# Optimization experiments

Measured on AMD Instinct MI355X. Metric: run time of the kernel, lower is better.

The kernel has to match this reference:

```python
import jax, jax.numpy as jnp
import numpy as np

D = 128          # embedding_dim
H = 8            # attention heads
DH = D // H      # per-head dim
SPLIT = 50000    # hyper-edge zero rows prepended
NX = 150000      # input node feature rows
N0 = SPLIT + NX  # layer-0 source nodes
N1 = 50000       # layer-0 targets
N2 = 30000       # layer-1 targets
N3 = 10000       # layer-2 targets
E0, E1, E2 = 500000, 300000, 100000
NTYPE = 65       # e_num + 1 edge types
NEG_SLOPE = 0.2
BETA = 0.5       # residual_beta (learn_beta=False)
BN_EPS = 1e-5

WEIGHT_NAMES = ['Wq0','Wk0','Wv0','Ws0','Wq1','Wk1','Wv1','Ws1','Wek1','Wev1','Wq2','Wk2','Wv2','Ws2']


def setup_inputs() -> dict:
    key = jax.random.key(0)
    ks = jax.random.split(key, 32)
    s = 1.0 / np.sqrt(D)
    inp = {}
    inp['x'] = jax.random.normal(ks[0], (NX, D), jnp.float32)
    inp['type_table'] = jax.random.normal(ks[1], (NTYPE, D), jnp.float32) * s
    inp['attr_table'] = jax.random.normal(ks[2], (NTYPE, D), jnp.float32) * s
    for i, nm in enumerate(WEIGHT_NAMES):
        inp[nm] = jax.random.normal(ks[3 + i], (D, D), jnp.float32) * s
    inp['g0'] = jnp.ones((D,), jnp.float32)
    inp['b0'] = jnp.zeros((D,), jnp.float32)
    inp['src0'] = jax.random.randint(ks[20], (E0,), 0, N0)
    inp['dst0'] = jax.random.randint(ks[21], (E0,), 0, N1)
    inp['src1'] = jax.random.randint(ks[22], (E1,), 0, N1)
    inp['dst1'] = jax.random.randint(ks[23], (E1,), 0, N2)
    inp['src2'] = jax.random.randint(ks[24], (E2,), 0, N2)
    inp['dst2'] = jax.random.randint(ks[25], (E2,), 0, N3)
    inp['edge_type'] = jax.random.randint(ks[26], (E1,), 0, NTYPE)
    return inp


def _conv(x_src, x_tgt, src, dst, Wq, Wk, Wv, Ws, ek=None, ev=None):
    # HypergraphTransformer: multi-head attention over incoming edges per target.
    Nt = x_tgt.shape[0]
    q = (x_tgt @ Wq).reshape(Nt, H, DH)
    k = (x_src @ Wk)[src]            # [E, D] project at nodes, gather at edges
    v = (x_src @ Wv)[src]
    if ek is not None:
        k = k + ek
        v = v + ev
    k = k.reshape(-1, H, DH)
    v = v.reshape(-1, H, DH)
    logits = (q[dst] * k).sum(-1) / np.sqrt(DH)          # [E, H]
    logits = jnp.where(logits >= 0, logits, NEG_SLOPE * logits)
    m = jax.ops.segment_max(logits, dst, num_segments=Nt)
    m = jnp.where(jnp.isfinite(m), m, 0.0)
    a = jnp.exp(logits - m[dst])
    ssum = jax.ops.segment_sum(a, dst, num_segments=Nt)
    alpha = a / (ssum[dst] + 1e-16)                      # segment softmax
    out = jax.ops.segment_sum(alpha[..., None] * v, dst, num_segments=Nt)
    out = out.reshape(Nt, D)                             # concat head fusion
    return BETA * (x_tgt @ Ws) + (1.0 - BETA) * out      # gated residual


def _bn(h, g, b):
    mu = h.mean(0)
    var = h.var(0)   # biased, as torch BatchNorm1d uses for normalization in training
    return (h - mu) / jnp.sqrt(var + BN_EPS) * g + b


def reference(x, type_table, attr_table, Wq0, Wk0, Wv0, Ws0, Wq1, Wk1, Wv1, Ws1,
              Wek1, Wev1, Wq2, Wk2, Wv2, Ws2, g0, b0,
              src0, dst0, src1, dst1, src2, dst2, edge_type):
    # prepend split_idx zero rows for hyper-edge embeddings
    h = jnp.concatenate([jnp.zeros((SPLIT, D), x.dtype), x], axis=0)  # [N0, D]
    # idx 0: v2e + BatchNorm
    h = _conv(h, h[:N1], src0, dst0, Wq0, Wk0, Wv0, Ws0)
    h = _bn(h, g0, b0)
    # idx 1: E2EConvs[0] with edge_type/attr embeddings added to K/V
    ek = type_table[edge_type] @ Wek1
    ev = attr_table[edge_type] @ Wev1
    h = _conv(h, h[:N2], src1, dst1, Wq1, Wk1, Wv1, Ws1, ek=ek, ev=ev)
    # idx 2: e2rel (no edge embeddings)
    h = _conv(h, h[:N3], src2, dst2, Wq2, Wk2, Wv2, Ws2)
    return h
```

## Files before the change

kernel.cpp:

```cpp
#include <hip/hip_runtime.h>
#include <math.h>

#define DD 128
#define SPLIT 50000
#define NN1 50000
#define NN2 30000
#define NN3 10000
#define EE0 500000
#define EE1 300000
#define EE2 100000
#define EALL (EE0 + EE1 + EE2)
#define NALL (NN1 + NN2 + NN3)
#define B1 50000
#define B2 80000
#define NEG 0.2f

typedef __attribute__((ext_vector_type(8))) short bf16x8;
typedef __attribute__((ext_vector_type(4))) float f32x4;

static __device__ __forceinline__ unsigned short f2bf(float x) {
  unsigned u = __float_as_uint(x);
  unsigned r = (u + 0x7FFFu + ((u >> 16) & 1u)) >> 16;
  return (unsigned short)r;
}
static __device__ __forceinline__ float bf2f(unsigned short b) {
  return __uint_as_float(((unsigned)b) << 16);
}

__global__ __launch_bounds__(256) void hist_kernel(
    const int* __restrict__ dst0, const int* __restrict__ dst1,
    const int* __restrict__ dst2, int* __restrict__ counts)
{
  for (int e = blockIdx.x * 256 + threadIdx.x; e < EALL; e += gridDim.x * 256) {
    int d;
    if (e < EE0) d = dst0[e];
    else if (e < EE0 + EE1) d = B1 + dst1[e - EE0];
    else d = B2 + dst2[e - EE0 - EE1];
    atomicAdd(&counts[d], 1);
  }
}

__global__ __launch_bounds__(256) void scan1_kernel(
    const int* __restrict__ counts, int* __restrict__ rp1,
    int* __restrict__ partial, int n)
{
  __shared__ int s[256];
  int t = threadIdx.x;
  int i = blockIdx.x * 256 + t;
  int v = (i < n) ? counts[i] : 0;
  s[t] = v; __syncthreads();
  for (int off = 1; off < 256; off <<= 1) {
    int tv = (t >= off) ? s[t - off] : 0;
    __syncthreads();
    s[t] += tv;
    __syncthreads();
  }
  if (i < n) rp1[i] = s[t];
  if (t == 255) partial[blockIdx.x] = s[255];
}

__global__ __launch_bounds__(256) void scan2_kernel(int* __restrict__ partial, int nb)
{
  __shared__ int s[256];
  int t = threadIdx.x;
  int carry = 0;
  for (int base = 0; base < nb; base += 256) {
    int i = base + t;
    int v = (i < nb) ? partial[i] : 0;
    s[t] = v; __syncthreads();
    for (int off = 1; off < 256; off <<= 1) {
      int tv = (t >= off) ? s[t - off] : 0;
      __syncthreads();
      s[t] += tv;
      __syncthreads();
    }
    int ex = carry + ((t == 0) ? 0 : s[t - 1]);
    if (i < nb) partial[i] = ex;
    int tot = s[255];
    __syncthreads();
    carry += tot;
  }
}

__global__ __launch_bounds__(256) void scan3_kernel(
    int* __restrict__ rp, const int* __restrict__ partial, int n)
{
  int i = blockIdx.x * 256 + threadIdx.x;
  if (i < n) rp[i + 1] += partial[i >> 8];
  if (i == 0) rp[0] = 0;
}

__global__ __launch_bounds__(256) void fill_kernel(
    const int* __restrict__ dst0, const int* __restrict__ src0,
    const int* __restrict__ dst1, const int* __restrict__ src1,
    const int* __restrict__ dst2, const int* __restrict__ src2,
    const int* __restrict__ etyp, int* __restrict__ cursor,
    int* __restrict__ vals)
{
  for (int e = blockIdx.x * 256 + threadIdx.x; e < EALL; e += gridDim.x * 256) {
    int d, v;
    if (e < EE0) { d = dst0[e]; v = src0[e]; }
    else if (e < EE0 + EE1) {
      int k = e - EE0;
      d = B1 + dst1[k]; v = src1[k] | (etyp[k] << 17);
    } else {
      int k = e - EE0 - EE1;
      d = B2 + dst2[k]; v = src2[k];
    }
    int slot = atomicAdd(&cursor[d], 1);
    vals[slot] = v;
  }
}

struct W9 { const float* w[9]; };
__global__ __launch_bounds__(256) void wprep_kernel(W9 srcs, unsigned short* out)
{
  int m = blockIdx.y;
  const float* W = srcs.w[m];
  unsigned short* hi = out + (size_t)m * 32768;
  unsigned short* lo = hi + 16384;
  for (int i = blockIdx.x * 256 + threadIdx.x; i < 16384; i += gridDim.x * 256) {
    int k = i >> 7, c = i & 127;
    float a = W[i];
    unsigned short h = f2bf(a);
    hi[c * DD + k] = h;
    lo[c * DD + k] = f2bf(a - bf2f(h));
  }
}

__global__ __launch_bounds__(256) void agg0_kernel(
    const float* __restrict__ x, const int* __restrict__ rp,
    const int* __restrict__ vals, float* __restrict__ acc, float* __restrict__ deg)
{
  int d = blockIdx.x * 4 + (threadIdx.x >> 6);
  if (d >= NN1) return;
  int lane = threadIdx.x & 63;
  int l32 = lane & 31, half = lane >> 5;
  int beg = rp[d], end = rp[d + 1];
  const float4* x4 = (const float4*)x;
  float4 a0 = {0.f, 0.f, 0.f, 0.f}, a1 = {0.f, 0.f, 0.f, 0.f};
  int j = beg + half;
  for (; j + 2 < end; j += 4) {
    int s0 = vals[j], s1 = vals[j + 2];
    if (s0 >= SPLIT) {
      float4 v = x4[(size_t)(s0 - SPLIT) * 32 + l32];
      a0.x += v.x; a0.y += v.y; a0.z += v.z; a0.w += v.w;
    }
    if (s1 >= SPLIT) {
      float4 v = x4[(size_t)(s1 - SPLIT) * 32 + l32];
      a1.x += v.x; a1.y += v.y; a1.z += v.z; a1.w += v.w;
    }
  }
  if (j < end) {
    int s0 = vals[j];
    if (s0 >= SPLIT) {
      float4 v = x4[(size_t)(s0 - SPLIT) * 32 + l32];
      a0.x += v.x; a0.y += v.y; a0.z += v.z; a0.w += v.w;
    }
  }
  a0.x += a1.x; a0.y += a1.y; a0.z += a1.z; a0.w += a1.w;
  a0.x += __shfl(a0.x, l32 + 32);
  a0.y += __shfl(a0.y, l32 + 32);
  a0.z += __shfl(a0.z, l32 + 32);
  a0.w += __shfl(a0.w, l32 + 32);
  if (half == 0) {
    ((float4*)acc)[(size_t)d * 32 + l32] = a0;
    if (l32 == 0) deg[d] = (float)(end - beg);
  }
}

__global__ __launch_bounds__(256) void gemm128_kernel(
    const float* __restrict__ A, const float* __restrict__ W,
    float* __restrict__ C, int N, const float* __restrict__ deg)
{
  __shared__ float Al[64 * 128];
  __shared__ float Wl[64 * 128];
  int t = threadIdx.x;
  int cg = t & 31;
  int rg = t >> 5;
  int r0 = blockIdx.x << 6;
  int nrows = N - r0; if (nrows > 64) nrows = 64;

  const float4* Ag = (const float4*)(A + (size_t)r0 * DD);
  float4* Al4 = (float4*)Al;
  for (int i = t; i < nrows * 32; i += 256) Al4[i] = Ag[i];

  float acc[8][4] = {};
  const float4* W4 = (const float4*)W;
  float4* Wl4 = (float4*)Wl;
  const float4* Al4c = (const float4*)Al;

  for (int half = 0; half < 2; ++half) {
    __syncthreads();
    for (int i = t; i < 2048; i += 256) Wl4[i] = W4[half * 2048 + i];
    __syncthreads();
    const float4* Wl4c = (const float4*)Wl;
    int kb4 = half * 16;
    for (int k4 = 0; k4 < 16; ++k4) {
      float4 w0 = Wl4c[(k4 * 4 + 0) * 32 + cg];
      float4 w1 = Wl4c[(k4 * 4 + 1) * 32 + cg];
      float4 w2 = Wl4c[(k4 * 4 + 2) * 32 + cg];
      float4 w3 = Wl4c[(k4 * 4 + 3) * 32 + cg];
#pragma unroll
      for (int r = 0; r < 8; ++r) {
        float4 a = Al4c[(rg * 8 + r) * 32 + kb4 + k4];
        acc[r][0] = fmaf(a.x, w0.x, acc[r][0]);
        acc[r][1] = fmaf(a.x, w0.y, acc[r][1]);
        acc[r][2] = fmaf(a.x, w0.z, acc[r][2]);
        acc[r][3] = fmaf(a.x, w0.w, acc[r][3]);
        acc[r][0] = fmaf(a.y, w1.x, acc[r][0]);
        acc[r][1] = fmaf(a.y, w1.y, acc[r][1]);
        acc[r][2] = fmaf(a.y, w1.z, acc[r][2]);
        acc[r][3] = fmaf(a.y, w1.w, acc[r][3]);
        acc[r][0] = fmaf(a.z, w2.x, acc[r][0]);
        acc[r][1] = fmaf(a.z, w2.y, acc[r][1]);
        acc[r][2] = fmaf(a.z, w2.z, acc[r][2]);
        acc[r][3] = fmaf(a.z, w2.w, acc[r][3]);
        acc[r][0] = fmaf(a.w, w3.x, acc[r][0]);
        acc[r][1] = fmaf(a.w, w3.y, acc[r][1]);
        acc[r][2] = fmaf(a.w, w3.z, acc[r][2]);
        acc[r][3] = fmaf(a.w, w3.w, acc[r][3]);
      }
    }
  }

#pragma unroll
  for (int r = 0; r < 8; ++r) {
    int rr = rg * 8 + r;
    if (rr < nrows) {
      float sc = 1.0f;
      if (deg) sc = 0.5f / (deg[r0 + rr] + 1e-16f);
      float4 o;
      o.x = acc[r][0] * sc; o.y = acc[r][1] * sc;
      o.z = acc[r][2] * sc; o.w = acc[r][3] * sc;
      ((float4*)(C + (size_t)(r0 + rr) * DD))[cg] = o;
    }
  }
}

__global__ __launch_bounds__(256) void mfma_gemm4_kernel(
    const float* __restrict__ A,
    const float* __restrict__ SC, const float* __restrict__ SH,
    const unsigned short* __restrict__ WP,
    int w0, int w1, int w2, int w3,
    float* __restrict__ C0, float* __restrict__ C1,
    float* __restrict__ C2, float* __restrict__ C3,
    int N0, int N1, int N2, int N3,
    const float* __restrict__ deg)
{
  int t = threadIdx.x;
  int l = t & 63;
  int wl = t >> 6;
  int r0 = blockIdx.x << 6;
  int rbase = r0 + wl * 16 + (l & 15);
  int r_ld = rbase < N0 ? rbase : (N0 - 1);
  int kg = (l >> 4) << 3;

  bf16x8 Ah[4], Al[4];
#pragma unroll
  for (int ks = 0; ks < 4; ++ks) {
    int k0 = ks * 32 + kg;
    const float4* ap = (const float4*)(A + (size_t)r_ld * DD + k0);
    float4 x0 = ap[0], x1 = ap[1];
    float av[8] = {x0.x, x0.y, x0.z, x0.w, x1.x, x1.y, x1.z, x1.w};
    if (SC) {
      const float4* scp = (const float4*)(SC + k0);
      const float4* shp = (const float4*)(SH + k0);
      float4 s0 = scp[0], s1 = scp[1], h0 = shp[0], h1 = shp[1];
      av[0] = fmaf(av[0], s0.x, h0.x);
      av[1] = fmaf(av[1], s0.y, h0.y);
      av[2] = fmaf(av[2], s0.z, h0.z);
      av[3] = fmaf(av[3], s0.w, h0.w);
      av[4] = fmaf(av[4], s1.x, h1.x);
      av[5] = fmaf(av[5], s1.y, h1.y);
      av[6] = fmaf(av[6], s1.z, h1.z);
      av[7] = fmaf(av[7], s1.w, h1.w);
    }
#pragma unroll
    for (int j = 0; j < 8; ++j) {
      unsigned short h = f2bf(av[j]);
      Ah[ks][j] = (short)h;
      Al[ks][j] = (short)f2bf(av[j] - bf2f(h));
    }
  }

  auto do_out = [&](int widx, float* C, int N, bool useDeg) {
    if (widx < 0 || r0 >= N) return;
    const unsigned short* Wh = WP + (size_t)widx * 32768;
    const unsigned short* Wl = Wh + 16384;
    f32x4 acc[8];
#pragma unroll
    for (int ct = 0; ct < 8; ++ct) acc[ct] = (f32x4){0.f, 0.f, 0.f, 0.f};
#pragma unroll
    for (int ks = 0; ks < 4; ++ks) {
      int koff = ks * 32 + kg;
#pragma unroll
      for (int ct = 0; ct < 8; ++ct) {
        int col = ct * 16 + (l & 15);
        bf16x8 bh = *(const bf16x8*)(Wh + (size_t)col * DD + koff);
        bf16x8 bl = *(const bf16x8*)(Wl + (size_t)col * DD + koff);
        acc[ct] = __builtin_amdgcn_mfma_f32_16x16x32_bf16(Ah[ks], bh, acc[ct], 0, 0, 0);
        acc[ct] = __builtin_amdgcn_mfma_f32_16x16x32_bf16(Al[ks], bh, acc[ct], 0, 0, 0);
        acc[ct] = __builtin_amdgcn_mfma_f32_16x16x32_bf16(Ah[ks], bl, acc[ct], 0, 0, 0);
      }
    }
    int rw = r0 + wl * 16 + ((l >> 4) << 2);
    float scl[4] = {1.f, 1.f, 1.f, 1.f};
    if (useDeg) {
#pragma unroll
      for (int r = 0; r < 4; ++r) {
        int rr = rw + r; if (rr > N - 1) rr = N - 1;
        scl[r] = 0.5f / (deg[rr] + 1e-16f);
      }
    }
#pragma unroll
    for (int ct = 0; ct < 8; ++ct) {
      int col = ct * 16 + (l & 15);
#pragma unroll
      for (int r = 0; r < 4; ++r) {
        int row = rw + r;
        if (row < N) C[(size_t)row * DD + col] = acc[ct][r] * scl[r];
      }
    }
  };

  do_out(w0, C0, N0, deg != nullptr);
  do_out(w1, C1, N1, false);
  do_out(w2, C2, N2, false);
  do_out(w3, C3, N3, false);
}

__global__ __launch_bounds__(256) void bn_stats_kernel(
    const float* __restrict__ H, float* __restrict__ sums)
{
  int t = threadIdx.x;
  int col = t & 127;
  float s = 0.f, q = 0.f;
  for (int r = blockIdx.x * 2 + (t >> 7); r < NN1; r += gridDim.x * 2) {
    float v = H[(size_t)r * DD + col];
    s += v; q += v * v;
  }
  __shared__ float ls[256], lq[256];
  ls[t] = s; lq[t] = q;
  __syncthreads();
  if (t < 128) {
    atomicAdd(&sums[col], ls[t] + ls[t + 128]);
    atomicAdd(&sums[128 + col], lq[t] + lq[t + 128]);
  }
}

__global__ __launch_bounds__(128) void bn_finalize_kernel(
    const float* __restrict__ sums, const float* __restrict__ g,
    const float* __restrict__ b, float* __restrict__ SC, float* __restrict__ SH)
{
  int c = threadIdx.x;
  const float invN = 1.0f / (float)NN1;
  float mu = sums[c] * invN;
  float var = sums[128 + c] * invN - mu * mu;
  float rs = rsqrtf(var + 1e-5f);
  float sc = rs * g[c];
  SC[c] = sc;
  SH[c] = b[c] - mu * sc;
}

__global__ __launch_bounds__(256) void attn_kernel(
    const float* __restrict__ Q, const float* __restrict__ K,
    const float* __restrict__ V, const float* __restrict__ EKT,
    const float* __restrict__ EVT, const int* __restrict__ rp,
    const int* __restrict__ vals, const float* __restrict__ Spre,
    float* __restrict__ Out, int Nt)
{
  int d = blockIdx.x * 4 + (threadIdx.x >> 6);
  if (d >= Nt) return;
  int lane = threadIdx.x & 63;
  int l32 = lane & 31, half = lane >> 5;

  const float4* Q4 = (const float4*)Q;
  const float4* K4 = (const float4*)K;
  const float4* V4 = (const float4*)V;
  float4 q = Q4[(size_t)d * 32 + l32];

  float m = -INFINITY, ss = 0.f;
  float4 o = {0.f, 0.f, 0.f, 0.f};

  int beg = rp[d], end = rp[d + 1];
  for (int j = beg + half; j < end; j += 2) {
    int pv = vals[j];
    float4 kk, vv;
    if (EKT) {
      int s = pv & 0x1FFFF, ty = pv >> 17;
      kk = K4[(size_t)s * 32 + l32];
      vv = V4[(size_t)s * 32 + l32];
      float4 ek = ((const float4*)EKT)[(size_t)ty * 32 + l32];
      float4 ev = ((const float4*)EVT)[(size_t)ty * 32 + l32];
      kk.x += ek.x; kk.y += ek.y; kk.z += ek.z; kk.w += ek.w;
      vv.x += ev.x; vv.y += ev.y; vv.z += ev.z; vv.w += ev.w;
    } else {
      kk = K4[(size_t)pv * 32 + l32];
      vv = V4[(size_t)pv * 32 + l32];
    }
    float p = q.x * kk.x + q.y * kk.y + q.z * kk.z + q.w * kk.w;
    p += __shfl_xor(p, 1);
    p += __shfl_xor(p, 2);
    float lg = p * 0.25f;
    lg = (lg >= 0.f) ? lg : NEG * lg;
    float nm = fmaxf(m, lg);
    float w = __expf(m - nm);
    float a = __expf(lg - nm);
    ss = ss * w + a;
    o.x = o.x * w + a * vv.x;
    o.y = o.y * w + a * vv.y;
    o.z = o.z * w + a * vv.z;
    o.w = o.w * w + a * vv.w;
    m = nm;
  }

  float mp = __shfl_xor(m, 32);
  float sp = __shfl_xor(ss, 32);
  float4 op;
  op.x = __shfl_xor(o.x, 32);
  op.y = __shfl_xor(o.y, 32);
  op.z = __shfl_xor(o.z, 32);
  op.w = __shfl_xor(o.w, 32);
  float nm = fmaxf(m, mp);
  if (nm == -INFINITY) nm = 0.f;
  float w = __expf(m - nm);
  float wp = __expf(mp - nm);
  float sT = ss * w + sp * wp;
  float inv = 1.0f / (sT + 1e-16f);
  float4 res;
  res.x = (o.x * w + op.x * wp) * inv;
  res.y = (o.y * w + op.y * wp) * inv;
  res.z = (o.z * w + op.z * wp) * inv;
  res.w = (o.w * w + op.w * wp) * inv;

  if (half == 0) {
    float4 sr = ((const float4*)Spre)[(size_t)d * 32 + l32];
    float4 ot;
    ot.x = 0.5f * (sr.x + res.x);
    ot.y = 0.5f * (sr.y + res.y);
    ot.z = 0.5f * (sr.z + res.z);
    ot.w = 0.5f * (sr.w + res.w);
    ((float4*)Out)[(size_t)d * 32 + l32] = ot;
  }
}

extern "C" void kernel_launch(void* const* d_in, const int* in_sizes, int n_in,
                              void* d_out, int out_size, void* d_ws, size_t ws_size,
                              hipStream_t stream)
{
  const float* x   = (const float*)d_in[0];
  const float* tt  = (const float*)d_in[1];
  const float* at  = (const float*)d_in[2];
  const float* Wv0 = (const float*)d_in[5];
  const float* Wq1 = (const float*)d_in[7];
  const float* Wk1 = (const float*)d_in[8];
  const float* Wv1 = (const float*)d_in[9];
  const float* Ws1 = (const float*)d_in[10];
  const float* Wek1= (const float*)d_in[11];
  const float* Wev1= (const float*)d_in[12];
  const float* Wq2 = (const float*)d_in[13];
  const float* Wk2 = (const float*)d_in[14];
  const float* Wv2 = (const float*)d_in[15];
  const float* Ws2 = (const float*)d_in[16];
  const float* g0  = (const float*)d_in[17];
  const float* b0  = (const float*)d_in[18];
  const int* src0 = (const int*)d_in[19];
  const int* dst0 = (const int*)d_in[20];
  const int* src1 = (const int*)d_in[21];
  const int* dst1 = (const int*)d_in[22];
  const int* src2 = (const int*)d_in[23];
  const int* dst2 = (const int*)d_in[24];
  const int* etyp = (const int*)d_in[25];

  float* ws = (float*)d_ws;

  const size_t O_K1  = 0;
  const size_t O_V1  = 6400000;
  const size_t O_Q1  = 12800000;
  const size_t O_H2  = 16640000;
  const size_t O_DEG = 20480000;
  const size_t O_EK  = 20530000;
  const size_t O_EV  = 20538320;
  const size_t O_BN  = 20546640;
  const size_t O_SC  = 20546896;
  const size_t O_SH  = 20547024;
  const size_t O_H1  = 20547152;
  const size_t O_K2  = 0;
  const size_t O_V2  = 3840000;
  const size_t O_Q2  = 7680000;
  const size_t O_S2  = 8960000;
  int* wi   = (int*)(ws + 26947152);
  int* RP   = wi;
  int* VALS = wi + 90001;
  int* CNT  = wi + 990001;
  int* PART = wi + 1080001;
  unsigned short* WPREP = (unsigned short*)(wi + 1080520);

  W9 w9;
  w9.w[0] = Wv0;
  w9.w[1] = Wk1; w9.w[2] = Wv1; w9.w[3] = Wq1; w9.w[4] = Ws1;
  w9.w[5] = Wk2; w9.w[6] = Wv2; w9.w[7] = Wq2; w9.w[8] = Ws2;
  wprep_kernel<<<dim3(8, 9), 256, 0, stream>>>(w9, WPREP);

  hipMemsetAsync(CNT, 0, (size_t)NALL * 4, stream);
  hist_kernel<<<3516, 256, 0, stream>>>(dst0, dst1, dst2, CNT);
  int nb = (NALL + 255) / 256;
  scan1_kernel<<<nb, 256, 0, stream>>>(CNT, RP + 1, PART, NALL);
  scan2_kernel<<<1, 256, 0, stream>>>(PART, nb);
  scan3_kernel<<<nb, 256, 0, stream>>>(RP, PART, NALL);
  hipMemcpyAsync(CNT, RP, (size_t)NALL * 4, hipMemcpyDeviceToDevice, stream);
  fill_kernel<<<3516, 256, 0, stream>>>(dst0, src0, dst1, src1, dst2, src2,
                                        etyp, CNT, VALS);

  hipMemsetAsync(ws + O_BN, 0, (size_t)256 * 4, stream);

  agg0_kernel<<<(NN1 + 3) / 4, 256, 0, stream>>>(x, RP, VALS, ws + O_K1, ws + O_DEG);
  mfma_gemm4_kernel<<<(NN1 + 63) / 64, 256, 0, stream>>>(
      ws + O_K1, nullptr, nullptr, WPREP,
      0, -1, -1, -1,
      ws + O_H1, nullptr, nullptr, nullptr,
      NN1, 0, 0, 0, ws + O_DEG);
  bn_stats_kernel<<<512, 256, 0, stream>>>(ws + O_H1, ws + O_BN);
  bn_finalize_kernel<<<1, 128, 0, stream>>>(ws + O_BN, g0, b0, ws + O_SC, ws + O_SH);

  mfma_gemm4_kernel<<<(NN1 + 63) / 64, 256, 0, stream>>>(
      ws + O_H1, ws + O_SC, ws + O_SH, WPREP,
      1, 2, 3, 4,
      ws + O_K1, ws + O_V1, ws + O_Q1, ws + O_H2,
      NN1, NN1, NN2, NN2, nullptr);
  gemm128_kernel<<<2, 256, 0, stream>>>(tt, Wek1, ws + O_EK, 65, nullptr);
  gemm128_kernel<<<2, 256, 0, stream>>>(at, Wev1, ws + O_EV, 65, nullptr);

  attn_kernel<<<(NN2 + 3) / 4, 256, 0, stream>>>(
      ws + O_Q1, ws + O_K1, ws + O_V1, ws + O_EK, ws + O_EV,
      RP + B1, VALS, ws + O_H2, ws + O_H2, NN2);

  mfma_gemm4_kernel<<<(NN2 + 63) / 64, 256, 0, stream>>>(
      ws + O_H2, nullptr, nullptr, WPREP,
      5, 6, 7, 8,
      ws + O_K2, ws + O_V2, ws + O_Q2, ws + O_S2,
      NN2, NN2, NN3, NN3, nullptr);

  attn_kernel<<<(NN3 + 3) / 4, 256, 0, stream>>>(
      ws + O_Q2, ws + O_K2, ws + O_V2, nullptr, nullptr,
      RP + B2, VALS, ws + O_S2, (float*)d_out, NN3);

  (void)in_sizes; (void)n_in; (void)out_size; (void)ws_size;
}
```

Before: 606.8 us.

## Split multi-output MFMA GEMM across grid y and unroll agg0 gather loop

The fused four-output GEMM kernel is replaced by one whose grid y dimension picks the output, and optionally a column-tile slice, so each block computes a single projection. Operands are swapped in the MFMA so each lane holds four contiguous columns and can write them as one vector store. The agg0 gather loop is unrolled to four loads per iteration, using branchless masked FMAs so the loads can be issued together. The aim is more parallelism, better store coalescing and more memory-level parallelism, at the cost of converting and loading A redundantly in every block along y.

```diff
diff --git a/kernel.cpp b/kernel.cpp
--- a/kernel.cpp
+++ b/kernel.cpp
@@ -140,18 +140,27 @@
   const float4* x4 = (const float4*)x;
   float4 a0 = {0.f, 0.f, 0.f, 0.f}, a1 = {0.f, 0.f, 0.f, 0.f};
   int j = beg + half;
-  for (; j + 2 < end; j += 4) {
-    int s0 = vals[j], s1 = vals[j + 2];
-    if (s0 >= SPLIT) {
-      float4 v = x4[(size_t)(s0 - SPLIT) * 32 + l32];
-      a0.x += v.x; a0.y += v.y; a0.z += v.z; a0.w += v.w;
-    }
-    if (s1 >= SPLIT) {
-      float4 v = x4[(size_t)(s1 - SPLIT) * 32 + l32];
-      a1.x += v.x; a1.y += v.y; a1.z += v.z; a1.w += v.w;
-    }
-  }
-  if (j < end) {
+  for (; j + 6 < end; j += 8) {
+    int s0 = vals[j], s1 = vals[j + 2], s2 = vals[j + 4], s3 = vals[j + 6];
+    int i0 = s0 - SPLIT, i1 = s1 - SPLIT, i2 = s2 - SPLIT, i3 = s3 - SPLIT;
+    float m0 = i0 >= 0 ? 1.f : 0.f; i0 = i0 >= 0 ? i0 : 0;
+    float m1 = i1 >= 0 ? 1.f : 0.f; i1 = i1 >= 0 ? i1 : 0;
+    float m2 = i2 >= 0 ? 1.f : 0.f; i2 = i2 >= 0 ? i2 : 0;
+    float m3 = i3 >= 0 ? 1.f : 0.f; i3 = i3 >= 0 ? i3 : 0;
+    float4 v0 = x4[(size_t)i0 * 32 + l32];
+    float4 v1 = x4[(size_t)i1 * 32 + l32];
+    float4 v2 = x4[(size_t)i2 * 32 + l32];
+    float4 v3 = x4[(size_t)i3 * 32 + l32];
+    a0.x = fmaf(m0, v0.x, a0.x); a0.y = fmaf(m0, v0.y, a0.y);
+    a0.z = fmaf(m0, v0.z, a0.z); a0.w = fmaf(m0, v0.w, a0.w);
+    a1.x = fmaf(m1, v1.x, a1.x); a1.y = fmaf(m1, v1.y, a1.y);
+    a1.z = fmaf(m1, v1.z, a1.z); a1.w = fmaf(m1, v1.w, a1.w);
+    a0.x = fmaf(m2, v2.x, a0.x); a0.y = fmaf(m2, v2.y, a0.y);
+    a0.z = fmaf(m2, v2.z, a0.z); a0.w = fmaf(m2, v2.w, a0.w);
+    a1.x = fmaf(m3, v3.x, a1.x); a1.y = fmaf(m3, v3.y, a1.y);
+    a1.z = fmaf(m3, v3.z, a1.z); a1.w = fmaf(m3, v3.w, a1.w);
+  }
+  for (; j < end; j += 2) {
     int s0 = vals[j];
     if (s0 >= SPLIT) {
       float4 v = x4[(size_t)(s0 - SPLIT) * 32 + l32];
@@ -238,22 +247,27 @@
   }
 }
 
-__global__ __launch_bounds__(256) void mfma_gemm4_kernel(
+struct GemmOuts { int widx[4]; float* C[4]; int N[4]; };
+__global__ __launch_bounds__(256) void mfma_gemm_kernel(
     const float* __restrict__ A,
     const float* __restrict__ SC, const float* __restrict__ SH,
     const unsigned short* __restrict__ WP,
-    int w0, int w1, int w2, int w3,
-    float* __restrict__ C0, float* __restrict__ C1,
-    float* __restrict__ C2, float* __restrict__ C3,
-    int N0, int N1, int N2, int N3,
+    GemmOuts outs, int tilesPerOut, int ctPerBlock,
     const float* __restrict__ deg)
 {
+  int out = blockIdx.y / tilesPerOut;
+  int N = outs.N[out];
+  int r0 = blockIdx.x << 6;
+  if (r0 >= N) return;
+  float* C = outs.C[out];
+  int ctOff = (blockIdx.y % tilesPerOut) * ctPerBlock;
+
   int t = threadIdx.x;
   int l = t & 63;
   int wl = t >> 6;
-  int r0 = blockIdx.x << 6;
-  int rbase = r0 + wl * 16 + (l & 15);
-  int r_ld = rbase < N0 ? rbase : (N0 - 1);
+  int l15 = l & 15;
+  int rbase = r0 + wl * 16 + l15;
+  int r_ld = rbase < N ? rbase : (N - 1);
   int kg = (l >> 4) << 3;
 
   bf16x8 Ah[4], Al[4];
@@ -284,50 +298,46 @@
     }
   }
 
-  auto do_out = [&](int widx, float* C, int N, bool useDeg) {
-    if (widx < 0 || r0 >= N) return;
-    const unsigned short* Wh = WP + (size_t)widx * 32768;
-    const unsigned short* Wl = Wh + 16384;
-    f32x4 acc[8];
-#pragma unroll
-    for (int ct = 0; ct < 8; ++ct) acc[ct] = (f32x4){0.f, 0.f, 0.f, 0.f};
-#pragma unroll
-    for (int ks = 0; ks < 4; ++ks) {
-      int koff = ks * 32 + kg;
-#pragma unroll
-      for (int ct = 0; ct < 8; ++ct) {
-        int col = ct * 16 + (l & 15);
-        bf16x8 bh = *(const bf16x8*)(Wh + (size_t)col * DD + koff);
-        bf16x8 bl = *(const bf16x8*)(Wl + (size_t)col * DD + koff);
-        acc[ct] = __builtin_amdgcn_mfma_f32_16x16x32_bf16(Ah[ks], bh, acc[ct], 0, 0, 0);
-        acc[ct] = __builtin_amdgcn_mfma_f32_16x16x32_bf16(Al[ks], bh, acc[ct], 0, 0, 0);
-        acc[ct] = __builtin_amdgcn_mfma_f32_16x16x32_bf16(Ah[ks], bl, acc[ct], 0, 0, 0);
-      }
-    }
-    int rw = r0 + wl * 16 + ((l >> 4) << 2);
-    float scl[4] = {1.f, 1.f, 1.f, 1.f};
-    if (useDeg) {
-#pragma unroll
-      for (int r = 0; r < 4; ++r) {
-        int rr = rw + r; if (rr > N - 1) rr = N - 1;
-        scl[r] = 0.5f / (deg[rr] + 1e-16f);
-      }
-    }
-#pragma unroll
-    for (int ct = 0; ct < 8; ++ct) {
-      int col = ct * 16 + (l & 15);
-#pragma unroll
-      for (int r = 0; r < 4; ++r) {
-        int row = rw + r;
-        if (row < N) C[(size_t)row * DD + col] = acc[ct][r] * scl[r];
-      }
-    }
-  };
-
-  do_out(w0, C0, N0, deg != nullptr);
-  do_out(w1, C1, N1, false);
-  do_out(w2, C2, N2, false);
-  do_out(w3, C3, N3, false);
+  const unsigned short* Wh = WP + (size_t)outs.widx[out] * 32768;
+  const unsigned short* Wl = Wh + 16384;
+
+  float dsc = 1.0f;
+  if (deg && out == 0) dsc = 0.5f / (deg[r_ld] + 1e-16f);
+  bool doStore = rbase < N;
+
+  for (int ct = 0; ct < ctPerBlock; ++ct) {
+    int col = (ctOff + ct) * 16 + l15;
+    const unsigned short* whp = Wh + (size_t)col * DD + kg;
+    const unsigned short* wlp = Wl + (size_t)col * DD + kg;
+    bf16x8 bh0 = *(const bf16x8*)(whp);
+    bf16x8 bh1 = *(const bf16x8*)(whp + 32);
+    bf16x8 bh2 = *(const bf16x8*)(whp + 64);
+    bf16x8 bh3 = *(const bf16x8*)(whp + 96);
+    bf16x8 bl0 = *(const bf16x8*)(wlp);
+    bf16x8 bl1 = *(const bf16x8*)(wlp + 32);
+    bf16x8 bl2 = *(const bf16x8*)(wlp + 64);
+    bf16x8 bl3 = *(const bf16x8*)(wlp + 96);
+    f32x4 acc = (f32x4){0.f, 0.f, 0.f, 0.f};
+    acc = __builtin_amdgcn_mfma_f32_16x16x32_bf16(bh0, Ah[0], acc, 0, 0, 0);
+    acc = __builtin_amdgcn_mfma_f32_16x16x32_bf16(bl0, Ah[0], acc, 0, 0, 0);
+    acc = __builtin_amdgcn_mfma_f32_16x16x32_bf16(bh0, Al[0], acc, 0, 0, 0);
+    acc = __builtin_amdgcn_mfma_f32_16x16x32_bf16(bh1, Ah[1], acc, 0, 0, 0);
+    acc = __builtin_amdgcn_mfma_f32_16x16x32_bf16(bl1, Ah[1], acc, 0, 0, 0);
+    acc = __builtin_amdgcn_mfma_f32_16x16x32_bf16(bh1, Al[1], acc, 0, 0, 0);
+    acc = __builtin_amdgcn_mfma_f32_16x16x32_bf16(bh2, Ah[2], acc, 0, 0, 0);
+    acc = __builtin_amdgcn_mfma_f32_16x16x32_bf16(bl2, Ah[2], acc, 0, 0, 0);
+    acc = __builtin_amdgcn_mfma_f32_16x16x32_bf16(bh2, Al[2], acc, 0, 0, 0);
+    acc = __builtin_amdgcn_mfma_f32_16x16x32_bf16(bh3, Ah[3], acc, 0, 0, 0);
+    acc = __builtin_amdgcn_mfma_f32_16x16x32_bf16(bl3, Ah[3], acc, 0, 0, 0);
+    acc = __builtin_amdgcn_mfma_f32_16x16x32_bf16(bh3, Al[3], acc, 0, 0, 0);
+    if (doStore) {
+      int colbase = (ctOff + ct) * 16 + ((l >> 4) << 2);
+      f32x4 o;
+      o[0] = acc[0] * dsc; o[1] = acc[1] * dsc;
+      o[2] = acc[2] * dsc; o[3] = acc[3] * dsc;
+      *(f32x4*)(C + (size_t)rbase * DD + colbase) = o;
+    }
+  }
 }
 
 __global__ __launch_bounds__(256) void bn_stats_kernel(
@@ -516,19 +526,24 @@
   hipMemsetAsync(ws + O_BN, 0, (size_t)256 * 4, stream);
 
   agg0_kernel<<<(NN1 + 3) / 4, 256, 0, stream>>>(x, RP, VALS, ws + O_K1, ws + O_DEG);
-  mfma_gemm4_kernel<<<(NN1 + 63) / 64, 256, 0, stream>>>(
-      ws + O_K1, nullptr, nullptr, WPREP,
-      0, -1, -1, -1,
-      ws + O_H1, nullptr, nullptr, nullptr,
-      NN1, 0, 0, 0, ws + O_DEG);
+  {
+    GemmOuts o{};
+    o.widx[0] = 0; o.C[0] = ws + O_H1; o.N[0] = NN1;
+    mfma_gemm_kernel<<<dim3((NN1 + 63) / 64, 2), 256, 0, stream>>>(
+        ws + O_K1, nullptr, nullptr, WPREP, o, 2, 4, ws + O_DEG);
+  }
   bn_stats_kernel<<<512, 256, 0, stream>>>(ws + O_H1, ws + O_BN);
   bn_finalize_kernel<<<1, 128, 0, stream>>>(ws + O_BN, g0, b0, ws + O_SC, ws + O_SH);
 
-  mfma_gemm4_kernel<<<(NN1 + 63) / 64, 256, 0, stream>>>(
-      ws + O_H1, ws + O_SC, ws + O_SH, WPREP,
-      1, 2, 3, 4,
-      ws + O_K1, ws + O_V1, ws + O_Q1, ws + O_H2,
-      NN1, NN1, NN2, NN2, nullptr);
+  {
+    GemmOuts o{};
+    o.widx[0] = 1; o.C[0] = ws + O_K1; o.N[0] = NN1;
+    o.widx[1] = 2; o.C[1] = ws + O_V1; o.N[1] = NN1;
+    o.widx[2] = 3; o.C[2] = ws + O_Q1; o.N[2] = NN2;
+    o.widx[3] = 4; o.C[3] = ws + O_H2; o.N[3] = NN2;
+    mfma_gemm_kernel<<<dim3((NN1 + 63) / 64, 4), 256, 0, stream>>>(
+        ws + O_H1, ws + O_SC, ws + O_SH, WPREP, o, 1, 8, nullptr);
+  }
   gemm128_kernel<<<2, 256, 0, stream>>>(tt, Wek1, ws + O_EK, 65, nullptr);
   gemm128_kernel<<<2, 256, 0, stream>>>(at, Wev1, ws + O_EV, 65, nullptr);
 
@@ -536,11 +551,15 @@
       ws + O_Q1, ws + O_K1, ws + O_V1, ws + O_EK, ws + O_EV,
       RP + B1, VALS, ws + O_H2, ws + O_H2, NN2);
 
-  mfma_gemm4_kernel<<<(NN2 + 63) / 64, 256, 0, stream>>>(
-      ws + O_H2, nullptr, nullptr, WPREP,
-      5, 6, 7, 8,
-      ws + O_K2, ws + O_V2, ws + O_Q2, ws + O_S2,
-      NN2, NN2, NN3, NN3, nullptr);
+  {
+    GemmOuts o{};
+    o.widx[0] = 5; o.C[0] = ws + O_K2; o.N[0] = NN2;
+    o.widx[1] = 6; o.C[1] = ws + O_V2; o.N[1] = NN2;
+    o.widx[2] = 7; o.C[2] = ws + O_Q2; o.N[2] = NN3;
+    o.widx[3] = 8; o.C[3] = ws + O_S2; o.N[3] = NN3;
+    mfma_gemm_kernel<<<dim3((NN2 + 63) / 64, 4), 256, 0, stream>>>(
+        ws + O_H2, nullptr, nullptr, WPREP, o, 1, 8, nullptr);
+  }
 
   attn_kernel<<<(NN3 + 3) / 4, 256, 0, stream>>>(
       ws + O_Q2, ws + O_K2, ws + O_V2, nullptr, nullptr,
```

Measured after the change: 602.0 us. No clear change (-0.8%).
